# Performance work log

Measured on AMD Instinct MI355X. Metric: run time of the kernel, lower is better.

The kernel has to match this reference:

```python
import jax, jax.numpy as jnp
import numpy as np

B, IN, HID, OUT, G = 16384, 1024, 2048, 256, 8


def _linear_init(key, fan_in, shape):
    bound = 1.0 / np.sqrt(fan_in)
    return jax.random.uniform(key, shape, jnp.float32, -bound, bound)


def setup_inputs() -> dict:
    key = jax.random.key(0)
    ks = jax.random.split(key, 10)
    x = jax.random.normal(ks[0], (B, IN), jnp.float32)
    gid = jax.random.randint(ks[1], (B,), 0, G)
    # stacked per-group head params (out_heads + final_out)
    W1 = _linear_init(ks[2], IN, (G, IN, HID))
    b1 = _linear_init(ks[3], IN, (G, HID))
    W2 = _linear_init(ks[4], HID, (G, HID, OUT))
    b2 = _linear_init(ks[5], HID, (G, OUT))
    # generic_out params
    Wg1 = _linear_init(ks[6], IN, (IN, HID))
    bg1 = _linear_init(ks[7], IN, (HID,))
    Wg2 = _linear_init(ks[8], HID, (HID, OUT))
    bg2 = _linear_init(ks[9], HID, (OUT,))
    return {"x": x, "gid": gid, "W1": W1, "b1": b1, "W2": W2, "b2": b2,
            "Wg1": Wg1, "bg1": bg1, "Wg2": Wg2, "bg2": bg2}


def reference(x, gid, W1, b1, W2, b2, Wg1, bg1, Wg2, bg2):
    # generic path (applied to every sample, as in the torch loop)
    gen_out = jax.nn.relu(x @ Wg1 + bg1) @ Wg2 + bg2  # [B, OUT]
    # routed path: loop over the small fixed number of groups (grouped-GEMM style),
    # selecting each sample's result by its group id.
    out = jnp.zeros_like(gen_out)
    for g in range(W1.shape[0]):
        h = jax.nn.relu(x @ W1[g] + b1[g])         # [B, HID]
        o = h @ W2[g] + b2[g]                       # [B, OUT]
        out = jnp.where((gid == g)[:, None], o, out)
    return out, gen_out
```

## Files before the change

kernel.cpp:

```cpp
#include <hip/hip_runtime.h>
#include <cstdint>
#include <cstddef>

static constexpr int Bn   = 16384;
static constexpr int INn  = 1024;
static constexpr int HIDn = 2048;
static constexpr int OUTn = 256;
static constexpr int NGn  = 8;
static constexpr int MAXT = 136;
static constexpr int NBLK = Bn / 256;

typedef __attribute__((ext_vector_type(8))) __bf16 bf16x8;
typedef __attribute__((ext_vector_type(4))) float  f32x4;

__device__ __forceinline__ unsigned short f2bf(float f) {
  unsigned int u = __builtin_bit_cast(unsigned int, f);
  u += 0x7fffu + ((u >> 16) & 1u);
  return (unsigned short)(u >> 16);
}

__device__ __forceinline__ void load_lds16(const void* g, void* l) {
  __builtin_amdgcn_global_load_lds(
      (const __attribute__((address_space(1))) unsigned int*)g,
      (__attribute__((address_space(3))) unsigned int*)l, 16, 0, 0);
}

__global__ void blkhist_k(const int* __restrict__ gid, int* __restrict__ blk_cnt) {
  __shared__ int h[NGn];
  if (threadIdx.x < NGn) h[threadIdx.x] = 0;
  __syncthreads();
  atomicAdd(&h[gid[blockIdx.x * 256 + threadIdx.x]], 1);
  __syncthreads();
  if (threadIdx.x < NGn) blk_cnt[blockIdx.x * NGn + threadIdx.x] = h[threadIdx.x];
}

__global__ void scan_desc_k(const int* __restrict__ blk_cnt, int* __restrict__ cnt,
                            int* __restrict__ goff, int* __restrict__ ntl,
                            int2* __restrict__ desc, int* __restrict__ bbase) {
  __shared__ int s[NGn][NBLK];
  __shared__ int tot[NGn], go[NGn];
  int t = threadIdx.x;
  int g = t >> 6, b = t & 63;
  s[g][b] = blk_cnt[b * NGn + g];
  __syncthreads();
  int pre = 0;
  for (int b2 = 0; b2 < b; b2++) pre += s[g][b2];
  if (b == 63) tot[g] = pre + s[g][63];
  __syncthreads();
  if (t == 0) {
    int o = 0, nt = 0;
    for (int gg = 0; gg < NGn; gg++) {
      go[gg] = o; goff[gg] = o; cnt[gg] = tot[gg];
      for (int m = 0; m < tot[gg]; m += 128) { desc[nt].x = gg; desc[nt].y = m; nt++; }
      o += tot[gg];
    }
    *ntl = nt;
  }
  __syncthreads();
  bbase[b * NGn + g] = go[g] + pre;
}

__global__ void place_k(const int* __restrict__ gid, const int* __restrict__ bbase,
                        int* __restrict__ ridx) {
  __shared__ int wcnt[4][NGn];
  int i = blockIdx.x * 256 + threadIdx.x;
  int g = gid[i];
  int lane = threadIdx.x & 63, w = threadIdx.x >> 6;
  unsigned long long mym = 0;
  #pragma unroll
  for (int grp = 0; grp < NGn; grp++) {
    unsigned long long m = __ballot(g == grp);
    if (lane == 0) wcnt[w][grp] = __popcll(m);
    if (g == grp) mym = m;
  }
  __syncthreads();
  int wrank = __popcll(mym & ((1ull << lane) - 1ull));
  int base = 0;
  for (int w2 = 0; w2 < w; w2++) base += wcnt[w2][g];
  ridx[bbase[blockIdx.x * NGn + g] + base + wrank] = i;
}

__global__ void conv_bf16_k(const float* __restrict__ src, unsigned short* __restrict__ dst,
                            int nvec) {
  int i = blockIdx.x * blockDim.x + threadIdx.x;
  int stride = gridDim.x * blockDim.x;
  for (; i < nvec; i += stride) {
    float4 v = ((const float4*)src)[i];
    uint2 o;
    o.x = (unsigned)f2bf(v.x) | ((unsigned)f2bf(v.y) << 16);
    o.y = (unsigned)f2bf(v.z) | ((unsigned)f2bf(v.w) << 16);
    ((uint2*)dst)[i] = o;
  }
}

__global__ void transpose_k(const float* __restrict__ src, unsigned short* __restrict__ dst,
                            int K, int N) {
  __shared__ float t[32][33];
  size_t bo = (size_t)blockIdx.z * (size_t)K * (size_t)N;
  int n0 = blockIdx.x * 32, k0 = blockIdx.y * 32;
  #pragma unroll
  for (int i = 0; i < 32; i += 8)
    t[threadIdx.y + i][threadIdx.x] =
        src[bo + (size_t)(k0 + threadIdx.y + i) * N + n0 + threadIdx.x];
  __syncthreads();
  #pragma unroll
  for (int i = 0; i < 32; i += 8)
    dst[bo + (size_t)(n0 + threadIdx.y + i) * K + k0 + threadIdx.x] =
        f2bf(t[threadIdx.x][threadIdx.y + i]);
}

template <bool GROUPED, bool GATHER_A, int OMODE>
__device__ __forceinline__ void gemm_body(
    const unsigned short* __restrict__ A, const unsigned short* __restrict__ Bt,
    const float* __restrict__ bias, void* __restrict__ Cout, int K, int N,
    int ksplit, size_t zstride,
    const int* __restrict__ cnt, const int* __restrict__ goff,
    const int* __restrict__ ntiles, const int2* __restrict__ desc,
    const int* __restrict__ ridx) {
  int mtile, ntile;
  {
    int gx = gridDim.x;
    int nwg = gx * gridDim.y;
    int l = blockIdx.y * gx + blockIdx.x;
    int q = nwg >> 3, rm = nwg & 7;
    int xcd = l & 7, i = l >> 3;
    int sl = (xcd < rm ? xcd * (q + 1) : rm * (q + 1) + (xcd - rm) * q) + i;
    mtile = sl / gx; ntile = sl - mtile * gx;
  }

  int row0, cnt_rem;
  if constexpr (GROUPED) {
    if (mtile >= *ntiles) return;
    int2 d = desc[mtile];
    int g = d.x;
    row0 = goff[g] + d.y;
    cnt_rem = cnt[g] - d.y;
    Bt += (size_t)g * (size_t)K * (size_t)N;
    if constexpr (OMODE == 0) bias += (size_t)g * (size_t)N;
  } else {
    row0 = mtile * 128;
    cnt_rem = 128;
  }
  int n0 = ntile * 128;
  const int kbase = blockIdx.z * ksplit;

  __shared__ __align__(16) char lds[32768];

  int t = threadIdx.x;
  int lane = t & 63, wid = t >> 6;

  const unsigned short* pA[4];
  const unsigned short* pB[4];
  #pragma unroll
  for (int i = 0; i < 4; i++) {
    int r = i * 32 + (t >> 3);
    int cg = (t & 7) ^ (r & 7);
    int rA;
    if constexpr (GROUPED) {
      int rcl = r < cnt_rem ? r : cnt_rem - 1;
      if constexpr (GATHER_A) rA = ridx[row0 + rcl];
      else                    rA = row0 + rcl;
    } else {
      rA = row0 + r;
    }
    pA[i] = A + (size_t)rA * K + cg * 8;
    pB[i] = Bt + (size_t)(n0 + r) * K + cg * 8;
  }

  int ln15 = lane & 15, l16 = lane >> 4, ln7 = lane & 7;
  int wm = wid >> 1, wn = wid & 1;
  int aoffb[4], boffb[4];
  #pragma unroll
  for (int m = 0; m < 4; m++) aoffb[m] = (wm * 64 + m * 16 + ln15) << 7;
  #pragma unroll
  for (int n = 0; n < 4; n++) boffb[n] = ((wn * 64 + n * 16 + ln15) << 7) + 16384;
  const int gsw0 = (l16 ^ ln7) << 4;
  const int gsw1 = ((4 + l16) ^ ln7) << 4;

  f32x4 acc[4][4];
  #pragma unroll
  for (int m = 0; m < 4; m++)
    #pragma unroll
    for (int n = 0; n < 4; n++) acc[m][n] = {0.f, 0.f, 0.f, 0.f};

  for (int kt = kbase; kt < kbase + ksplit; kt += 64) {
    __syncthreads();
    #pragma unroll
    for (int i = 0; i < 4; i++)
      load_lds16(pA[i] + kt, lds + i * 4096 + wid * 1024);
    #pragma unroll
    for (int i = 0; i < 4; i++)
      load_lds16(pB[i] + kt, lds + 16384 + i * 4096 + wid * 1024);
    __syncthreads();
    #pragma unroll
    for (int ks = 0; ks < 2; ks++) {
      const int gsw = ks ? gsw1 : gsw0;
      bf16x8 av[4], bv[4];
      #pragma unroll
      for (int m = 0; m < 4; m++) av[m] = *(const bf16x8*)(lds + aoffb[m] + gsw);
      #pragma unroll
      for (int n = 0; n < 4; n++) bv[n] = *(const bf16x8*)(lds + boffb[n] + gsw);
      #pragma unroll
      for (int m = 0; m < 4; m++)
        #pragma unroll
        for (int n = 0; n < 4; n++)
          acc[m][n] = __builtin_amdgcn_mfma_f32_16x16x32_bf16(av[m], bv[n], acc[m][n], 0, 0, 0);
    }
  }

  float biasv[4];
  if constexpr (OMODE == 0) {
    #pragma unroll
    for (int n = 0; n < 4; n++) biasv[n] = bias[n0 + wn * 64 + n * 16 + ln15];
  }
  float* Po = (float*)Cout + (size_t)blockIdx.z * zstride;

  #pragma unroll
  for (int m = 0; m < 4; m++) {
    #pragma unroll
    for (int j = 0; j < 4; j++) {
      int r = wm * 64 + m * 16 + l16 * 4 + j;
      if (GROUPED && r >= cnt_rem) continue;
      size_t orow = (size_t)(row0 + r);
      #pragma unroll
      for (int n = 0; n < 4; n++) {
        int col = n0 + wn * 64 + n * 16 + ln15;
        if constexpr (OMODE == 0) {
          float v = acc[m][n][j] + biasv[n];
          v = v > 0.f ? v : 0.f;
          ((unsigned short*)Cout)[orow * N + col] = f2bf(v);
        } else {
          Po[orow * N + col] = acc[m][n][j];
        }
      }
    }
  }
}

__global__ __launch_bounds__(256, 2) void g1gen_k(
    const unsigned short* A, const unsigned short* Bt, const float* bias, void* C,
    int K, int N, int ksplit, size_t zs,
    const int* cnt, const int* goff, const int* ntl, const int2* desc, const int* ridx) {
  gemm_body<false, false, 0>(A, Bt, bias, C, K, N, ksplit, zs, cnt, goff, ntl, desc, ridx);
}
__global__ __launch_bounds__(256, 2) void g1rt_k(
    const unsigned short* A, const unsigned short* Bt, const float* bias, void* C,
    int K, int N, int ksplit, size_t zs,
    const int* cnt, const int* goff, const int* ntl, const int2* desc, const int* ridx) {
  gemm_body<true, true, 0>(A, Bt, bias, C, K, N, ksplit, zs, cnt, goff, ntl, desc, ridx);
}
__global__ __launch_bounds__(256, 2) void g2gen_k(
    const unsigned short* A, const unsigned short* Bt, const float* bias, void* C,
    int K, int N, int ksplit, size_t zs,
    const int* cnt, const int* goff, const int* ntl, const int2* desc, const int* ridx) {
  gemm_body<false, false, 1>(A, Bt, bias, C, K, N, ksplit, zs, cnt, goff, ntl, desc, ridx);
}
__global__ __launch_bounds__(256, 2) void g2rt_k(
    const unsigned short* A, const unsigned short* Bt, const float* bias, void* C,
    int K, int N, int ksplit, size_t zs,
    const int* cnt, const int* goff, const int* ntl, const int2* desc, const int* ridx) {
  gemm_body<true, false, 1>(A, Bt, bias, C, K, N, ksplit, zs, cnt, goff, ntl, desc, ridx);
}

__global__ void redu_gen_k(const float* __restrict__ P, const float* __restrict__ bias,
                           float* __restrict__ outp) {
  int i = blockIdx.x * 256 + threadIdx.x;
  float4 a = ((const float4*)P)[i];
  float4 b = ((const float4*)(P + (size_t)Bn * OUTn))[i];
  int c4 = (i & 63) << 2;
  float4 bv = *(const float4*)(bias + c4);
  ((float4*)outp)[i] = {a.x + b.x + bv.x, a.y + b.y + bv.y,
                        a.z + b.z + bv.z, a.w + b.w + bv.w};
}

__global__ void redu_rt_k(const float* __restrict__ P, const float* __restrict__ b2,
                          float* __restrict__ outp,
                          const int* __restrict__ cnt, const int* __restrict__ goff,
                          const int* __restrict__ ntl, const int2* __restrict__ desc,
                          const int* __restrict__ ridx) {
  if ((int)blockIdx.x >= *ntl) return;
  int2 d = desc[blockIdx.x];
  int g = d.x;
  int row0 = goff[g] + d.y;
  int rem = cnt[g] - d.y; if (rem > 128) rem = 128;
  int t = threadIdx.x;
  int c4 = (t & 63) << 2;
  float4 bv = *(const float4*)(b2 + (size_t)g * OUTn + c4);
  for (int r = t >> 6; r < rem; r += 4) {
    size_t src = (size_t)(row0 + r) * OUTn + c4;
    float4 a = *(const float4*)(P + src);
    float4 b = *(const float4*)(P + (size_t)Bn * OUTn + src);
    int orow = ridx[row0 + r];
    *(float4*)(outp + (size_t)orow * OUTn + c4) =
        {a.x + b.x + bv.x, a.y + b.y + bv.y, a.z + b.z + bv.z, a.w + b.w + bv.w};
  }
}

extern "C" void kernel_launch(void* const* d_in, const int* in_sizes, int n_in,
                              void* d_out, int out_size, void* d_ws, size_t ws_size,
                              hipStream_t stream) {
  const float* x   = (const float*)d_in[0];
  const int*   gid = (const int*)d_in[1];
  const float* W1  = (const float*)d_in[2];
  const float* b1  = (const float*)d_in[3];
  const float* W2  = (const float*)d_in[4];
  const float* b2  = (const float*)d_in[5];
  const float* Wg1 = (const float*)d_in[6];
  const float* bg1 = (const float*)d_in[7];
  const float* Wg2 = (const float*)d_in[8];
  const float* bg2 = (const float*)d_in[9];

  float* out = (float*)d_out;
  float* gen = out + (size_t)Bn * OUTn;

  char* ws = (char*)d_ws;
  unsigned short* xb   = (unsigned short*)(ws);
  unsigned short* W1t  = (unsigned short*)(ws + 33554432);
  float*          Ppar = (float*)(ws + 33554432);
  unsigned short* W2t  = (unsigned short*)(ws + 67108864);
  unsigned short* Wg1t = (unsigned short*)(ws + 75497472);
  unsigned short* Wg2t = (unsigned short*)(ws + 79691776);
  unsigned short* h    = (unsigned short*)(ws + 80740352);
  int* ridx            = (int*)(ws + 147849216);
  int* meta            = (int*)(ws + 147914752);
  int* cnt  = meta;
  int* goff = meta + 8;
  int* ntl  = meta + 16;
  int2* desc = (int2*)(meta + 32);
  int* blk_cnt = meta + 512;
  int* bbase   = meta + 1024;

  const size_t zstr = (size_t)Bn * OUTn;

  blkhist_k<<<NBLK, 256, 0, stream>>>(gid, blk_cnt);
  scan_desc_k<<<1, 512, 0, stream>>>(blk_cnt, cnt, goff, ntl, desc, bbase);
  place_k<<<NBLK, 256, 0, stream>>>(gid, bbase, ridx);

  conv_bf16_k<<<2048, 256, 0, stream>>>(x, xb, Bn * INn / 4);
  dim3 tb(32, 8);
  transpose_k<<<dim3(HIDn / 32, INn / 32, NGn), tb, 0, stream>>>(W1, W1t, INn, HIDn);
  transpose_k<<<dim3(OUTn / 32, HIDn / 32, NGn), tb, 0, stream>>>(W2, W2t, HIDn, OUTn);
  transpose_k<<<dim3(HIDn / 32, INn / 32, 1), tb, 0, stream>>>(Wg1, Wg1t, INn, HIDn);
  transpose_k<<<dim3(OUTn / 32, HIDn / 32, 1), tb, 0, stream>>>(Wg2, Wg2t, HIDn, OUTn);

  g1rt_k<<<dim3(HIDn / 128, MAXT), 256, 0, stream>>>(
      xb, W1t, b1, h, INn, HIDn, INn, 0, cnt, goff, ntl, desc, ridx);
  g2rt_k<<<dim3(OUTn / 128, MAXT, 2), 256, 0, stream>>>(
      h, W2t, nullptr, Ppar, HIDn, OUTn, HIDn / 2, zstr, cnt, goff, ntl, desc, ridx);
  redu_rt_k<<<MAXT, 256, 0, stream>>>(Ppar, b2, out, cnt, goff, ntl, desc, ridx);

  g1gen_k<<<dim3(HIDn / 128, Bn / 128), 256, 0, stream>>>(
      xb, Wg1t, bg1, h, INn, HIDn, INn, 0, nullptr, nullptr, nullptr, nullptr, nullptr);
  g2gen_k<<<dim3(OUTn / 128, Bn / 128, 2), 256, 0, stream>>>(
      h, Wg2t, nullptr, Ppar, HIDn, OUTn, HIDn / 2, zstr, nullptr, nullptr, nullptr, nullptr, nullptr);
  redu_gen_k<<<(Bn * OUTn / 4) / 256, 256, 0, stream>>>(Ppar, bg2, gen);
}
```

Measured before the change: 291.5 us.

## Replace first-layer GEMMs with 256x256-tile 8-wave ping-pong pipelined kernel

Adds a new first-layer GEMM kernel using 256x256 output tiles, 512 threads and a double-buffered LDS pipeline. Each K step is split into four quarter-phases that interleave global-to-LDS loads with MFMA batches under explicit barriers and priority hints. Both the routed (gather via ridx) and generic first layers now use it, and the scan kernel emits a second 256-row tile descriptor list for the routed case. The aim is higher operand reuse per LDS load and better overlap of memory with MFMA work. In exchange it needs 128KB of LDS per block and more registers, and routed groups get more padded rows in their last tile.

```diff
diff --git a/kernel.cpp b/kernel.cpp
--- a/kernel.cpp
+++ b/kernel.cpp
@@ -8,6 +8,7 @@
 static constexpr int OUTn = 256;
 static constexpr int NGn  = 8;
 static constexpr int MAXT = 136;
+static constexpr int MAXT2 = 72;
 static constexpr int NBLK = Bn / 256;
 
 typedef __attribute__((ext_vector_type(8))) __bf16 bf16x8;
@@ -36,7 +37,9 @@
 
 __global__ void scan_desc_k(const int* __restrict__ blk_cnt, int* __restrict__ cnt,
                             int* __restrict__ goff, int* __restrict__ ntl,
-                            int2* __restrict__ desc, int* __restrict__ bbase) {
+                            int* __restrict__ ntl2,
+                            int2* __restrict__ desc, int2* __restrict__ desc256,
+                            int* __restrict__ bbase) {
   __shared__ int s[NGn][NBLK];
   __shared__ int tot[NGn], go[NGn];
   int t = threadIdx.x;
@@ -48,13 +51,14 @@
   if (b == 63) tot[g] = pre + s[g][63];
   __syncthreads();
   if (t == 0) {
-    int o = 0, nt = 0;
+    int o = 0, nt = 0, nt2 = 0;
     for (int gg = 0; gg < NGn; gg++) {
       go[gg] = o; goff[gg] = o; cnt[gg] = tot[gg];
       for (int m = 0; m < tot[gg]; m += 128) { desc[nt].x = gg; desc[nt].y = m; nt++; }
+      for (int m = 0; m < tot[gg]; m += 256) { desc256[nt2].x = gg; desc256[nt2].y = m; nt2++; }
       o += tot[gg];
     }
-    *ntl = nt;
+    *ntl = nt; *ntl2 = nt2;
   }
   __syncthreads();
   bbase[b * NGn + g] = go[g] + pre;
@@ -108,6 +112,227 @@
     dst[bo + (size_t)(n0 + threadIdx.y + i) * K + k0 + threadIdx.x] =
         f2bf(t[threadIdx.x][threadIdx.y + i]);
 }
+
+#define STAGE(U, KT, BUFP) do {                                        \
+    load_lds16(gp[(U)*2+0] + (KT)*64, (BUFP) + loff[(U)*2+0]);         \
+    load_lds16(gp[(U)*2+1] + (KT)*64, (BUFP) + loff[(U)*2+1]); } while (0)
+
+template <bool GROUPED>
+__global__ __launch_bounds__(512, 2) void g1_8ph_k(
+    const unsigned short* __restrict__ A, const unsigned short* __restrict__ Bt,
+    const float* __restrict__ bias, unsigned short* __restrict__ Cout,
+    const int* __restrict__ cnt, const int* __restrict__ goff,
+    const int* __restrict__ ntl2, const int2* __restrict__ desc256,
+    const int* __restrict__ ridx) {
+  constexpr int K = INn;
+  constexpr int N = HIDn;
+  constexpr int NT = K / 64;
+
+  int mtile, ntile;
+  {
+    int gx = gridDim.x;
+    int nwg = gx * gridDim.y;
+    int l = blockIdx.y * gx + blockIdx.x;
+    int q = nwg >> 3, rm = nwg & 7;
+    int xcd = l & 7, i = l >> 3;
+    int sl = (xcd < rm ? xcd * (q + 1) : rm * (q + 1) + (xcd - rm) * q) + i;
+    mtile = sl / gx; ntile = sl - mtile * gx;
+  }
+  int row0, cnt_rem;
+  if constexpr (GROUPED) {
+    if (mtile >= *ntl2) return;
+    int2 d = desc256[mtile];
+    int g = d.x;
+    row0 = goff[g] + d.y;
+    cnt_rem = cnt[g] - d.y;
+    Bt += (size_t)g * (size_t)K * (size_t)N;
+    bias += (size_t)g * N;
+  } else {
+    row0 = mtile * 256; cnt_rem = 256;
+  }
+  const int n0 = ntile * 256;
+
+  __shared__ __align__(16) char lds[131072];
+
+  const int t = threadIdx.x, lane = t & 63, wid = t >> 6;
+  const int wm = wid >> 2, wn = wid & 3;
+  const int ln15 = lane & 15, l16 = lane >> 4, ln7 = lane & 7;
+
+  const unsigned short* gp[8];
+  int loff[8];
+  #pragma unroll
+  for (int u = 0; u < 4; u++) {
+    #pragma unroll
+    for (int j = 0; j < 2; j++) {
+      int c = j * 512 + t;
+      int rl = c >> 3, gg = c & 7;
+      int r;
+      if (u == 0)      r = rl + ((rl & 64) ? 64 : 0);
+      else if (u == 1) r = 64 + rl + ((rl & 64) ? 64 : 0);
+      else {
+        r = ((rl >> 5) << 6) + (rl & 31);
+        if (u == 3) r += 32;
+      }
+      int gsrcg = gg ^ (r & 7);
+      if (u < 2) {
+        int rr;
+        if constexpr (GROUPED) {
+          int rc = r < cnt_rem ? r : cnt_rem - 1;
+          rr = ridx[row0 + rc];
+        } else rr = row0 + r;
+        gp[u * 2 + j] = A + (size_t)rr * K + gsrcg * 8;
+      } else {
+        gp[u * 2 + j] = Bt + (size_t)(n0 + r) * K + gsrcg * 8;
+      }
+      int rl0 = j * 64 + wid * 8;
+      int r0;
+      if (u == 0)      r0 = rl0 + ((rl0 & 64) ? 64 : 0);
+      else if (u == 1) r0 = 64 + rl0 + ((rl0 & 64) ? 64 : 0);
+      else {
+        r0 = ((rl0 >> 5) << 6) + (rl0 & 31);
+        if (u == 3) r0 += 32;
+      }
+      loff[u * 2 + j] = (u < 2 ? 0 : 32768) + r0 * 128;
+    }
+  }
+
+  int arow[8], brow[4];
+  #pragma unroll
+  for (int m = 0; m < 8; m++) arow[m] = (wm * 128 + m * 16 + ln15) << 7;
+  #pragma unroll
+  for (int n = 0; n < 4; n++) brow[n] = 32768 + ((wn * 64 + n * 16 + ln15) << 7);
+  const int g0 = (l16 ^ ln7) << 4;
+  const int g1 = ((4 + l16) ^ ln7) << 4;
+
+  f32x4 acc[8][4];
+  #pragma unroll
+  for (int m = 0; m < 8; m++)
+    #pragma unroll
+    for (int n = 0; n < 4; n++) acc[m][n] = {0.f, 0.f, 0.f, 0.f};
+
+  char* const buf0 = lds;
+  char* const buf1 = lds + 65536;
+
+  STAGE(0, 0, buf0); STAGE(2, 0, buf0); STAGE(3, 0, buf0); STAGE(1, 0, buf0);
+  STAGE(0, 1, buf1); STAGE(2, 1, buf1); STAGE(3, 1, buf1);
+  asm volatile("s_waitcnt vmcnt(6)" ::: "memory");
+  __builtin_amdgcn_s_barrier();
+
+  bf16x8 avL[4][2], avH[4][2], bvL[2][2], bvH[2][2];
+
+  auto KTILE = [&](int tt, char* bufc, char* bufn) {
+    const int kc1 = tt + 1 < NT ? tt + 1 : NT - 1;
+    const int kc2 = tt + 2 < NT ? tt + 2 : NT - 1;
+    #pragma unroll
+    for (int m = 0; m < 4; m++) {
+      avL[m][0] = *(const bf16x8*)(bufc + arow[m] + g0);
+      avL[m][1] = *(const bf16x8*)(bufc + arow[m] + g1);
+    }
+    #pragma unroll
+    for (int n = 0; n < 2; n++) {
+      bvL[n][0] = *(const bf16x8*)(bufc + brow[n] + g0);
+      bvL[n][1] = *(const bf16x8*)(bufc + brow[n] + g1);
+    }
+    STAGE(1, kc1, bufn);
+    __builtin_amdgcn_sched_barrier(0);
+    __builtin_amdgcn_s_barrier();
+    asm volatile("s_waitcnt lgkmcnt(0)" ::: "memory");
+    __builtin_amdgcn_sched_barrier(0);
+    __builtin_amdgcn_s_setprio(1);
+    #pragma unroll
+    for (int ks = 0; ks < 2; ks++)
+      #pragma unroll
+      for (int m = 0; m < 4; m++)
+        #pragma unroll
+        for (int n = 0; n < 2; n++)
+          acc[m][n] = __builtin_amdgcn_mfma_f32_16x16x32_bf16(avL[m][ks], bvL[n][ks], acc[m][n], 0, 0, 0);
+    __builtin_amdgcn_s_setprio(0);
+    __builtin_amdgcn_sched_barrier(0);
+    __builtin_amdgcn_s_barrier();
+    #pragma unroll
+    for (int n = 0; n < 2; n++) {
+      bvH[n][0] = *(const bf16x8*)(bufc + brow[2 + n] + g0);
+      bvH[n][1] = *(const bf16x8*)(bufc + brow[2 + n] + g1);
+    }
+    STAGE(0, kc2, bufc);
+    __builtin_amdgcn_sched_barrier(0);
+    __builtin_amdgcn_s_barrier();
+    asm volatile("s_waitcnt lgkmcnt(0)" ::: "memory");
+    __builtin_amdgcn_sched_barrier(0);
+    __builtin_amdgcn_s_setprio(1);
+    #pragma unroll
+    for (int ks = 0; ks < 2; ks++)
+      #pragma unroll
+      for (int m = 0; m < 4; m++)
+        #pragma unroll
+        for (int n = 0; n < 2; n++)
+          acc[m][2 + n] = __builtin_amdgcn_mfma_f32_16x16x32_bf16(avL[m][ks], bvH[n][ks], acc[m][2 + n], 0, 0, 0);
+    __builtin_amdgcn_s_setprio(0);
+    __builtin_amdgcn_sched_barrier(0);
+    __builtin_amdgcn_s_barrier();
+    #pragma unroll
+    for (int m = 0; m < 4; m++) {
+      avH[m][0] = *(const bf16x8*)(bufc + arow[4 + m] + g0);
+      avH[m][1] = *(const bf16x8*)(bufc + arow[4 + m] + g1);
+    }
+    STAGE(2, kc2, bufc);
+    __builtin_amdgcn_sched_barrier(0);
+    __builtin_amdgcn_s_barrier();
+    asm volatile("s_waitcnt lgkmcnt(0)" ::: "memory");
+    __builtin_amdgcn_sched_barrier(0);
+    __builtin_amdgcn_s_setprio(1);
+    #pragma unroll
+    for (int ks = 0; ks < 2; ks++)
+      #pragma unroll
+      for (int m = 0; m < 4; m++)
+        #pragma unroll
+        for (int n = 0; n < 2; n++)
+          acc[4 + m][2 + n] = __builtin_amdgcn_mfma_f32_16x16x32_bf16(avH[m][ks], bvH[n][ks], acc[4 + m][2 + n], 0, 0, 0);
+    __builtin_amdgcn_s_setprio(0);
+    __builtin_amdgcn_sched_barrier(0);
+    __builtin_amdgcn_s_barrier();
+    STAGE(3, kc2, bufc);
+    asm volatile("s_waitcnt vmcnt(6)" ::: "memory");
+    __builtin_amdgcn_sched_barrier(0);
+    __builtin_amdgcn_s_barrier();
+    __builtin_amdgcn_s_setprio(1);
+    #pragma unroll
+    for (int ks = 0; ks < 2; ks++)
+      #pragma unroll
+      for (int m = 0; m < 4; m++)
+        #pragma unroll
+        for (int n = 0; n < 2; n++)
+          acc[4 + m][n] = __builtin_amdgcn_mfma_f32_16x16x32_bf16(avH[m][ks], bvL[n][ks], acc[4 + m][n], 0, 0, 0);
+    __builtin_amdgcn_s_setprio(0);
+    __builtin_amdgcn_sched_barrier(0);
+    __builtin_amdgcn_s_barrier();
+  };
+
+  for (int it = 0; it < NT; it += 2) {
+    KTILE(it, buf0, buf1);
+    KTILE(it + 1, buf1, buf0);
+  }
+
+  float biasv[4];
+  #pragma unroll
+  for (int n = 0; n < 4; n++) biasv[n] = bias[n0 + wn * 64 + n * 16 + ln15];
+  #pragma unroll
+  for (int m = 0; m < 8; m++) {
+    #pragma unroll
+    for (int j = 0; j < 4; j++) {
+      int r = wm * 128 + m * 16 + l16 * 4 + j;
+      if (GROUPED && r >= cnt_rem) continue;
+      size_t orow = (size_t)(row0 + r);
+      #pragma unroll
+      for (int n = 0; n < 4; n++) {
+        float v = acc[m][n][j] + biasv[n];
+        v = v > 0.f ? v : 0.f;
+        Cout[orow * N + n0 + wn * 64 + n * 16 + ln15] = f2bf(v);
+      }
+    }
+  }
+}
+#undef STAGE
 
 template <bool GROUPED, bool GATHER_A, int OMODE>
 __device__ __forceinline__ void gemm_body(
@@ -237,18 +462,6 @@
   }
 }
 
-__global__ __launch_bounds__(256, 2) void g1gen_k(
-    const unsigned short* A, const unsigned short* Bt, const float* bias, void* C,
-    int K, int N, int ksplit, size_t zs,
-    const int* cnt, const int* goff, const int* ntl, const int2* desc, const int* ridx) {
-  gemm_body<false, false, 0>(A, Bt, bias, C, K, N, ksplit, zs, cnt, goff, ntl, desc, ridx);
-}
-__global__ __launch_bounds__(256, 2) void g1rt_k(
-    const unsigned short* A, const unsigned short* Bt, const float* bias, void* C,
-    int K, int N, int ksplit, size_t zs,
-    const int* cnt, const int* goff, const int* ntl, const int2* desc, const int* ridx) {
-  gemm_body<true, true, 0>(A, Bt, bias, C, K, N, ksplit, zs, cnt, goff, ntl, desc, ridx);
-}
 __global__ __launch_bounds__(256, 2) void g2gen_k(
     const unsigned short* A, const unsigned short* Bt, const float* bias, void* C,
     int K, int N, int ksplit, size_t zs,
@@ -323,17 +536,19 @@
   unsigned short* h    = (unsigned short*)(ws + 80740352);
   int* ridx            = (int*)(ws + 147849216);
   int* meta            = (int*)(ws + 147914752);
-  int* cnt  = meta;
-  int* goff = meta + 8;
-  int* ntl  = meta + 16;
-  int2* desc = (int2*)(meta + 32);
+  int* cnt   = meta;
+  int* goff  = meta + 8;
+  int* ntl   = meta + 16;
+  int* ntl2  = meta + 17;
+  int2* desc    = (int2*)(meta + 32);
+  int2* desc256 = (int2*)(meta + 304);
   int* blk_cnt = meta + 512;
   int* bbase   = meta + 1024;
 
   const size_t zstr = (size_t)Bn * OUTn;
 
   blkhist_k<<<NBLK, 256, 0, stream>>>(gid, blk_cnt);
-  scan_desc_k<<<1, 512, 0, stream>>>(blk_cnt, cnt, goff, ntl, desc, bbase);
+  scan_desc_k<<<1, 512, 0, stream>>>(blk_cnt, cnt, goff, ntl, ntl2, desc, desc256, bbase);
   place_k<<<NBLK, 256, 0, stream>>>(gid, bbase, ridx);
 
   conv_bf16_k<<<2048, 256, 0, stream>>>(x, xb, Bn * INn / 4);
@@ -343,14 +558,14 @@
   transpose_k<<<dim3(HIDn / 32, INn / 32, 1), tb, 0, stream>>>(Wg1, Wg1t, INn, HIDn);
   transpose_k<<<dim3(OUTn / 32, HIDn / 32, 1), tb, 0, stream>>>(Wg2, Wg2t, HIDn, OUTn);
 
-  g1rt_k<<<dim3(HIDn / 128, MAXT), 256, 0, stream>>>(
-      xb, W1t, b1, h, INn, HIDn, INn, 0, cnt, goff, ntl, desc, ridx);
+  g1_8ph_k<true><<<dim3(HIDn / 256, MAXT2), 512, 0, stream>>>(
+      xb, W1t, b1, h, cnt, goff, ntl2, desc256, ridx);
   g2rt_k<<<dim3(OUTn / 128, MAXT, 2), 256, 0, stream>>>(
       h, W2t, nullptr, Ppar, HIDn, OUTn, HIDn / 2, zstr, cnt, goff, ntl, desc, ridx);
   redu_rt_k<<<MAXT, 256, 0, stream>>>(Ppar, b2, out, cnt, goff, ntl, desc, ridx);
 
-  g1gen_k<<<dim3(HIDn / 128, Bn / 128), 256, 0, stream>>>(
-      xb, Wg1t, bg1, h, INn, HIDn, INn, 0, nullptr, nullptr, nullptr, nullptr, nullptr);
+  g1_8ph_k<false><<<dim3(HIDn / 256, Bn / 256), 512, 0, stream>>>(
+      xb, Wg1t, bg1, h, nullptr, nullptr, nullptr, nullptr, nullptr);
   g2gen_k<<<dim3(OUTn / 128, Bn / 128, 2), 256, 0, stream>>>(
       h, Wg2t, nullptr, Ppar, HIDn, OUTn, HIDn / 2, zstr, nullptr, nullptr, nullptr, nullptr, nullptr);
   redu_gen_k<<<(Bn * OUTn / 4) / 256, 256, 0, stream>>>(Ppar, bg2, gen);
```

After: 309.7 us. 6.2% more time.

## Merge routed and generic GEMMs, preprocessing and reductions into fewer launches

Applied to the files above, without the earlier changes.

Folds the bf16 conversion of x and the four weight transposes into a single kernel that dispatches on block index. When the workspace is large enough, the routed and generic GEMMs share one launch per layer, each with its own hidden buffer, so their tiles fill the device together. The two final reductions also become one kernel. The aim is to cut launch overhead and the partly idle tail waves of the separate kernels. The cost is a dependence on workspace size and a larger, mixed-work grid with more branching per block.

```diff
diff --git a/kernel.cpp b/kernel.cpp
--- a/kernel.cpp
+++ b/kernel.cpp
@@ -23,6 +23,13 @@
   __builtin_amdgcn_global_load_lds(
       (const __attribute__((address_space(1))) unsigned int*)g,
       (__attribute__((address_space(3))) unsigned int*)l, 16, 0, 0);
+}
+
+__device__ __forceinline__ void swz(int l, int nwg, int gx, int& mt, int& nt) {
+  int q = nwg >> 3, rm = nwg & 7;
+  int xcd = l & 7, i = l >> 3;
+  int sl = (xcd < rm ? xcd * (q + 1) : rm * (q + 1) + (xcd - rm) * q) + i;
+  mt = sl / gx; nt = sl - mt * gx;
 }
 
 __global__ void blkhist_k(const int* __restrict__ gid, int* __restrict__ blk_cnt) {
@@ -80,54 +87,66 @@
   ridx[bbase[blockIdx.x * NGn + g] + base + wrank] = i;
 }
 
-__global__ void conv_bf16_k(const float* __restrict__ src, unsigned short* __restrict__ dst,
-                            int nvec) {
-  int i = blockIdx.x * blockDim.x + threadIdx.x;
-  int stride = gridDim.x * blockDim.x;
-  for (; i < nvec; i += stride) {
-    float4 v = ((const float4*)src)[i];
-    uint2 o;
-    o.x = (unsigned)f2bf(v.x) | ((unsigned)f2bf(v.y) << 16);
-    o.y = (unsigned)f2bf(v.z) | ((unsigned)f2bf(v.w) << 16);
-    ((uint2*)dst)[i] = o;
-  }
-}
-
-__global__ void transpose_k(const float* __restrict__ src, unsigned short* __restrict__ dst,
-                            int K, int N) {
-  __shared__ float t[32][33];
-  size_t bo = (size_t)blockIdx.z * (size_t)K * (size_t)N;
-  int n0 = blockIdx.x * 32, k0 = blockIdx.y * 32;
+__global__ void convtrans_k(const float* __restrict__ x, unsigned short* __restrict__ xb,
+                            const float* __restrict__ W1, unsigned short* __restrict__ W1t,
+                            const float* __restrict__ W2, unsigned short* __restrict__ W2t,
+                            const float* __restrict__ Wg1, unsigned short* __restrict__ Wg1t,
+                            const float* __restrict__ Wg2, unsigned short* __restrict__ Wg2t) {
+  __shared__ float tlds[32][33];
+  int bx = blockIdx.x;
+  if (bx >= 23040) {
+    int t = threadIdx.y * 32 + threadIdx.x;
+    int i = (bx - 23040) * 256 + t;
+    const int nvec = Bn * INn / 4;
+    for (; i < nvec; i += 2048 * 256) {
+      float4 v = ((const float4*)x)[i];
+      uint2 o;
+      o.x = (unsigned)f2bf(v.x) | ((unsigned)f2bf(v.y) << 16);
+      o.y = (unsigned)f2bf(v.z) | ((unsigned)f2bf(v.w) << 16);
+      ((uint2*)xb)[i] = o;
+    }
+    return;
+  }
+  const float* src; unsigned short* dst;
+  int K, N, nx, ky; size_t bo;
+  if (bx < 16384) {
+    int z = bx >> 11, rem = bx & 2047;
+    nx = rem & 63; ky = rem >> 6; K = INn; N = HIDn;
+    src = W1; dst = W1t; bo = (size_t)z * K * N;
+  } else if (bx < 20480) {
+    int i2 = bx - 16384; int z = i2 >> 9, rem = i2 & 511;
+    nx = rem & 7; ky = rem >> 3; K = HIDn; N = OUTn;
+    src = W2; dst = W2t; bo = (size_t)z * K * N;
+  } else if (bx < 22528) {
+    int i3 = bx - 20480;
+    nx = i3 & 63; ky = i3 >> 6; K = INn; N = HIDn;
+    src = Wg1; dst = Wg1t; bo = 0;
+  } else {
+    int i4 = bx - 22528;
+    nx = i4 & 7; ky = i4 >> 3; K = HIDn; N = OUTn;
+    src = Wg2; dst = Wg2t; bo = 0;
+  }
+  int n0 = nx * 32, k0 = ky * 32;
   #pragma unroll
   for (int i = 0; i < 32; i += 8)
-    t[threadIdx.y + i][threadIdx.x] =
+    tlds[threadIdx.y + i][threadIdx.x] =
         src[bo + (size_t)(k0 + threadIdx.y + i) * N + n0 + threadIdx.x];
   __syncthreads();
   #pragma unroll
   for (int i = 0; i < 32; i += 8)
     dst[bo + (size_t)(n0 + threadIdx.y + i) * K + k0 + threadIdx.x] =
-        f2bf(t[threadIdx.x][threadIdx.y + i]);
+        f2bf(tlds[threadIdx.x][threadIdx.y + i]);
 }
 
 template <bool GROUPED, bool GATHER_A, int OMODE>
-__device__ __forceinline__ void gemm_body(
+__device__ __forceinline__ void gemm_tile(
+    int mtile, int ntile,
     const unsigned short* __restrict__ A, const unsigned short* __restrict__ Bt,
     const float* __restrict__ bias, void* __restrict__ Cout, int K, int N,
     int ksplit, size_t zstride,
     const int* __restrict__ cnt, const int* __restrict__ goff,
     const int* __restrict__ ntiles, const int2* __restrict__ desc,
     const int* __restrict__ ridx) {
-  int mtile, ntile;
-  {
-    int gx = gridDim.x;
-    int nwg = gx * gridDim.y;
-    int l = blockIdx.y * gx + blockIdx.x;
-    int q = nwg >> 3, rm = nwg & 7;
-    int xcd = l & 7, i = l >> 3;
-    int sl = (xcd < rm ? xcd * (q + 1) : rm * (q + 1) + (xcd - rm) * q) + i;
-    mtile = sl / gx; ntile = sl - mtile * gx;
-  }
-
   int row0, cnt_rem;
   if constexpr (GROUPED) {
     if (mtile >= *ntiles) return;
@@ -237,62 +256,107 @@
   }
 }
 
-__global__ __launch_bounds__(256, 2) void g1gen_k(
-    const unsigned short* A, const unsigned short* Bt, const float* bias, void* C,
-    int K, int N, int ksplit, size_t zs,
-    const int* cnt, const int* goff, const int* ntl, const int2* desc, const int* ridx) {
-  gemm_body<false, false, 0>(A, Bt, bias, C, K, N, ksplit, zs, cnt, goff, ntl, desc, ridx);
-}
+__global__ __launch_bounds__(256, 2) void g1both_k(
+    const unsigned short* xb, const unsigned short* W1t, const float* b1,
+    unsigned short* h_rt, const unsigned short* Wg1t, const float* bg1,
+    unsigned short* h_gen, const int* cnt, const int* goff, const int* ntl,
+    const int2* desc, const int* ridx) {
+  const int gx = HIDn / 128;
+  int mt, nt;
+  if ((int)blockIdx.y < MAXT) {
+    swz(blockIdx.y * gx + blockIdx.x, MAXT * gx, gx, mt, nt);
+    gemm_tile<true, true, 0>(mt, nt, xb, W1t, b1, h_rt, INn, HIDn, INn, 0,
+                             cnt, goff, ntl, desc, ridx);
+  } else {
+    swz((blockIdx.y - MAXT) * gx + blockIdx.x, (Bn / 128) * gx, gx, mt, nt);
+    gemm_tile<false, false, 0>(mt, nt, xb, Wg1t, bg1, h_gen, INn, HIDn, INn, 0,
+                               nullptr, nullptr, nullptr, nullptr, nullptr);
+  }
+}
+
+__global__ __launch_bounds__(256, 2) void g2both_k(
+    const unsigned short* h_rt, const unsigned short* W2t, float* Prt,
+    const unsigned short* h_gen, const unsigned short* Wg2t, float* Pgen,
+    const int* cnt, const int* goff, const int* ntl,
+    const int2* desc, const int* ridx) {
+  const int gx = OUTn / 128;
+  const size_t zstr = (size_t)Bn * OUTn;
+  int mt, nt;
+  if ((int)blockIdx.y < MAXT) {
+    swz(blockIdx.y * gx + blockIdx.x, MAXT * gx, gx, mt, nt);
+    gemm_tile<true, false, 1>(mt, nt, h_rt, W2t, nullptr, Prt, HIDn, OUTn,
+                              HIDn / 2, zstr, cnt, goff, ntl, desc, ridx);
+  } else {
+    swz((blockIdx.y - MAXT) * gx + blockIdx.x, (Bn / 128) * gx, gx, mt, nt);
+    gemm_tile<false, false, 1>(mt, nt, h_gen, Wg2t, nullptr, Pgen, HIDn, OUTn,
+                               HIDn / 2, zstr, nullptr, nullptr, nullptr, nullptr, nullptr);
+  }
+}
+
 __global__ __launch_bounds__(256, 2) void g1rt_k(
     const unsigned short* A, const unsigned short* Bt, const float* bias, void* C,
-    int K, int N, int ksplit, size_t zs,
     const int* cnt, const int* goff, const int* ntl, const int2* desc, const int* ridx) {
-  gemm_body<true, true, 0>(A, Bt, bias, C, K, N, ksplit, zs, cnt, goff, ntl, desc, ridx);
+  int mt, nt;
+  swz(blockIdx.y * gridDim.x + blockIdx.x, gridDim.x * gridDim.y, gridDim.x, mt, nt);
+  gemm_tile<true, true, 0>(mt, nt, A, Bt, bias, C, INn, HIDn, INn, 0,
+                           cnt, goff, ntl, desc, ridx);
+}
+__global__ __launch_bounds__(256, 2) void g1gen_k(
+    const unsigned short* A, const unsigned short* Bt, const float* bias, void* C) {
+  int mt, nt;
+  swz(blockIdx.y * gridDim.x + blockIdx.x, gridDim.x * gridDim.y, gridDim.x, mt, nt);
+  gemm_tile<false, false, 0>(mt, nt, A, Bt, bias, C, INn, HIDn, INn, 0,
+                             nullptr, nullptr, nullptr, nullptr, nullptr);
+}
+__global__ __launch_bounds__(256, 2) void g2rt_k(
+    const unsigned short* A, const unsigned short* Bt, float* P,
+    const int* cnt, const int* goff, const int* ntl, const int2* desc, const int* ridx) {
+  int mt, nt;
+  swz(blockIdx.y * gridDim.x + blockIdx.x, gridDim.x * gridDim.y, gridDim.x, mt, nt);
+  gemm_tile<true, false, 1>(mt, nt, A, Bt, nullptr, P, HIDn, OUTn, HIDn / 2,
+                            (size_t)Bn * OUTn, cnt, goff, ntl, desc, ridx);
 }
 __global__ __launch_bounds__(256, 2) void g2gen_k(
-    const unsigned short* A, const unsigned short* Bt, const float* bias, void* C,
-    int K, int N, int ksplit, size_t zs,
-    const int* cnt, const int* goff, const int* ntl, const int2* desc, const int* ridx) {
-  gemm_body<false, false, 1>(A, Bt, bias, C, K, N, ksplit, zs, cnt, goff, ntl, desc, ridx);
-}
-__global__ __launch_bounds__(256, 2) void g2rt_k(
-    const unsigned short* A, const unsigned short* Bt, const float* bias, void* C,
-    int K, int N, int ksplit, size_t zs,
-    const int* cnt, const int* goff, const int* ntl, const int2* desc, const int* ridx) {
-  gemm_body<true, false, 1>(A, Bt, bias, C, K, N, ksplit, zs, cnt, goff, ntl, desc, ridx);
-}
-
-__global__ void redu_gen_k(const float* __restrict__ P, const float* __restrict__ bias,
-                           float* __restrict__ outp) {
-  int i = blockIdx.x * 256 + threadIdx.x;
-  float4 a = ((const float4*)P)[i];
-  float4 b = ((const float4*)(P + (size_t)Bn * OUTn))[i];
-  int c4 = (i & 63) << 2;
-  float4 bv = *(const float4*)(bias + c4);
-  ((float4*)outp)[i] = {a.x + b.x + bv.x, a.y + b.y + bv.y,
-                        a.z + b.z + bv.z, a.w + b.w + bv.w};
-}
-
-__global__ void redu_rt_k(const float* __restrict__ P, const float* __restrict__ b2,
-                          float* __restrict__ outp,
-                          const int* __restrict__ cnt, const int* __restrict__ goff,
-                          const int* __restrict__ ntl, const int2* __restrict__ desc,
-                          const int* __restrict__ ridx) {
-  if ((int)blockIdx.x >= *ntl) return;
-  int2 d = desc[blockIdx.x];
-  int g = d.x;
-  int row0 = goff[g] + d.y;
-  int rem = cnt[g] - d.y; if (rem > 128) rem = 128;
+    const unsigned short* A, const unsigned short* Bt, float* P) {
+  int mt, nt;
+  swz(blockIdx.y * gridDim.x + blockIdx.x, gridDim.x * gridDim.y, gridDim.x, mt, nt);
+  gemm_tile<false, false, 1>(mt, nt, A, Bt, nullptr, P, HIDn, OUTn, HIDn / 2,
+                             (size_t)Bn * OUTn, nullptr, nullptr, nullptr, nullptr, nullptr);
+}
+
+__global__ void redu_k(const float* __restrict__ Pg, const float* __restrict__ Pr,
+                       const float* __restrict__ bg2, const float* __restrict__ b2,
+                       float* __restrict__ gen, float* __restrict__ outp,
+                       const int* __restrict__ cnt, const int* __restrict__ goff,
+                       const int* __restrict__ ntl, const int2* __restrict__ desc,
+                       const int* __restrict__ ridx) {
+  int bx = blockIdx.x;
   int t = threadIdx.x;
-  int c4 = (t & 63) << 2;
-  float4 bv = *(const float4*)(b2 + (size_t)g * OUTn + c4);
-  for (int r = t >> 6; r < rem; r += 4) {
-    size_t src = (size_t)(row0 + r) * OUTn + c4;
-    float4 a = *(const float4*)(P + src);
-    float4 b = *(const float4*)(P + (size_t)Bn * OUTn + src);
-    int orow = ridx[row0 + r];
-    *(float4*)(outp + (size_t)orow * OUTn + c4) =
-        {a.x + b.x + bv.x, a.y + b.y + bv.y, a.z + b.z + bv.z, a.w + b.w + bv.w};
+  if (bx < 4096) {
+    int i = bx * 256 + t;
+    float4 a = ((const float4*)Pg)[i];
+    float4 b = ((const float4*)(Pg + (size_t)Bn * OUTn))[i];
+    int c4 = (i & 63) << 2;
+    float4 bv = *(const float4*)(bg2 + c4);
+    ((float4*)gen)[i] = {a.x + b.x + bv.x, a.y + b.y + bv.y,
+                         a.z + b.z + bv.z, a.w + b.w + bv.w};
+  } else {
+    int bt = bx - 4096;
+    if (bt >= *ntl) return;
+    int2 d = desc[bt];
+    int g = d.x;
+    int row0 = goff[g] + d.y;
+    int rem = cnt[g] - d.y; if (rem > 128) rem = 128;
+    int c4 = (t & 63) << 2;
+    float4 bv = *(const float4*)(b2 + (size_t)g * OUTn + c4);
+    for (int r = t >> 6; r < rem; r += 4) {
+      size_t src = (size_t)(row0 + r) * OUTn + c4;
+      float4 a = *(const float4*)(Pr + src);
+      float4 b = *(const float4*)(Pr + (size_t)Bn * OUTn + src);
+      int orow = ridx[row0 + r];
+      *(float4*)(outp + (size_t)orow * OUTn + c4) =
+          {a.x + b.x + bv.x, a.y + b.y + bv.y, a.z + b.z + bv.z, a.w + b.w + bv.w};
+    }
   }
 }
 
@@ -314,44 +378,48 @@
   float* gen = out + (size_t)Bn * OUTn;
 
   char* ws = (char*)d_ws;
+  const bool big = ws_size >= 215100000ull;
+
   unsigned short* xb   = (unsigned short*)(ws);
+  float*          Pgen = (float*)(ws);
   unsigned short* W1t  = (unsigned short*)(ws + 33554432);
-  float*          Ppar = (float*)(ws + 33554432);
+  float*          Prt  = (float*)(ws + 33554432);
   unsigned short* W2t  = (unsigned short*)(ws + 67108864);
   unsigned short* Wg1t = (unsigned short*)(ws + 75497472);
   unsigned short* Wg2t = (unsigned short*)(ws + 79691776);
-  unsigned short* h    = (unsigned short*)(ws + 80740352);
-  int* ridx            = (int*)(ws + 147849216);
-  int* meta            = (int*)(ws + 147914752);
-  int* cnt  = meta;
-  int* goff = meta + 8;
-  int* ntl  = meta + 16;
+  unsigned short* h_rt = (unsigned short*)(ws + 80740352);
+  unsigned short* h_gen = big ? (unsigned short*)(ws + 147849216) : h_rt;
+  char* tail = big ? (ws + 214958080) : (ws + 147849216);
+  int* ridx = (int*)tail;
+  int* meta = (int*)(tail + 65536);
+  int* cnt   = meta;
+  int* goff  = meta + 8;
+  int* ntl   = meta + 16;
   int2* desc = (int2*)(meta + 32);
   int* blk_cnt = meta + 512;
   int* bbase   = meta + 1024;
 
-  const size_t zstr = (size_t)Bn * OUTn;
-
   blkhist_k<<<NBLK, 256, 0, stream>>>(gid, blk_cnt);
   scan_desc_k<<<1, 512, 0, stream>>>(blk_cnt, cnt, goff, ntl, desc, bbase);
   place_k<<<NBLK, 256, 0, stream>>>(gid, bbase, ridx);
 
-  conv_bf16_k<<<2048, 256, 0, stream>>>(x, xb, Bn * INn / 4);
-  dim3 tb(32, 8);
-  transpose_k<<<dim3(HIDn / 32, INn / 32, NGn), tb, 0, stream>>>(W1, W1t, INn, HIDn);
-  transpose_k<<<dim3(OUTn / 32, HIDn / 32, NGn), tb, 0, stream>>>(W2, W2t, HIDn, OUTn);
-  transpose_k<<<dim3(HIDn / 32, INn / 32, 1), tb, 0, stream>>>(Wg1, Wg1t, INn, HIDn);
-  transpose_k<<<dim3(OUTn / 32, HIDn / 32, 1), tb, 0, stream>>>(Wg2, Wg2t, HIDn, OUTn);
-
-  g1rt_k<<<dim3(HIDn / 128, MAXT), 256, 0, stream>>>(
-      xb, W1t, b1, h, INn, HIDn, INn, 0, cnt, goff, ntl, desc, ridx);
-  g2rt_k<<<dim3(OUTn / 128, MAXT, 2), 256, 0, stream>>>(
-      h, W2t, nullptr, Ppar, HIDn, OUTn, HIDn / 2, zstr, cnt, goff, ntl, desc, ridx);
-  redu_rt_k<<<MAXT, 256, 0, stream>>>(Ppar, b2, out, cnt, goff, ntl, desc, ridx);
-
-  g1gen_k<<<dim3(HIDn / 128, Bn / 128), 256, 0, stream>>>(
-      xb, Wg1t, bg1, h, INn, HIDn, INn, 0, nullptr, nullptr, nullptr, nullptr, nullptr);
-  g2gen_k<<<dim3(OUTn / 128, Bn / 128, 2), 256, 0, stream>>>(
-      h, Wg2t, nullptr, Ppar, HIDn, OUTn, HIDn / 2, zstr, nullptr, nullptr, nullptr, nullptr, nullptr);
-  redu_gen_k<<<(Bn * OUTn / 4) / 256, 256, 0, stream>>>(Ppar, bg2, gen);
-}
+  convtrans_k<<<25088, dim3(32, 8), 0, stream>>>(x, xb, W1, W1t, W2, W2t,
+                                                 Wg1, Wg1t, Wg2, Wg2t);
+
+  if (big) {
+    g1both_k<<<dim3(HIDn / 128, MAXT + Bn / 128), 256, 0, stream>>>(
+        xb, W1t, b1, h_rt, Wg1t, bg1, h_gen, cnt, goff, ntl, desc, ridx);
+    g2both_k<<<dim3(OUTn / 128, MAXT + Bn / 128, 2), 256, 0, stream>>>(
+        h_rt, W2t, Prt, h_gen, Wg2t, Pgen, cnt, goff, ntl, desc, ridx);
+  } else {
+    g1rt_k<<<dim3(HIDn / 128, MAXT), 256, 0, stream>>>(
+        xb, W1t, b1, h_rt, cnt, goff, ntl, desc, ridx);
+    g2rt_k<<<dim3(OUTn / 128, MAXT, 2), 256, 0, stream>>>(
+        h_rt, W2t, Prt, cnt, goff, ntl, desc, ridx);
+    g1gen_k<<<dim3(HIDn / 128, Bn / 128), 256, 0, stream>>>(xb, Wg1t, bg1, h_gen);
+    g2gen_k<<<dim3(OUTn / 128, Bn / 128, 2), 256, 0, stream>>>(h_gen, Wg2t, Pgen);
+  }
+
+  redu_k<<<4096 + MAXT, 256, 0, stream>>>(Pgen, Prt, bg2, b2, gen, out,
+                                          cnt, goff, ntl, desc, ridx);
+}
```

Result: slower. 328.0 us (+12.5%).
